# Kernel optimization log

Measured on AMD Instinct MI355X. Metric: run time of the kernel, lower is better.

## Reference

```python
import jax, jax.numpy as jnp
import numpy as np

M_GROUPS = 512  # fixed number of segments (== fill_max for ii)


def setup_inputs() -> dict:
    key = jax.random.key(0)
    ks = jax.random.split(key, 8)
    B, N, D = 4, 16384, 384
    x = jax.random.normal(ks[0], (B, N, D), dtype=jnp.float32)
    ii = jax.random.randint(ks[1], (N,), 0, M_GROUPS)
    s = 1.0 / np.sqrt(D)
    f_w = jax.random.uniform(ks[2], (D, D), jnp.float32, -s, s)
    f_b = jax.random.uniform(ks[3], (D,), jnp.float32, -s, s)
    g_w = jax.random.uniform(ks[4], (D, D), jnp.float32, -s, s)
    g_b = jax.random.uniform(ks[5], (D,), jnp.float32, -s, s)
    h_w = jax.random.uniform(ks[6], (D, D), jnp.float32, -s, s)
    h_b = jax.random.uniform(ks[7], (D,), jnp.float32, -s, s)
    return {"x": x, "ii": ii, "f_w": f_w, "f_b": f_b,
            "g_w": g_w, "g_b": g_b, "h_w": h_w, "h_b": h_b}


def reference(x, ii, f_w, f_b, g_w, g_b, h_w, h_b):
    # x: [B, N, D], ii: [N] group indices in [0, M_GROUPS)
    logits = x @ g_w.T + g_b                      # g(x): [B, N, D]
    exp_logits = jnp.exp(logits)
    # segment sum over n for each group m (== one-hot einsum 'bnm,bnd->bmd')
    seg = lambda e: jax.ops.segment_sum(e, ii, num_segments=M_GROUPS)
    sum_exp = jax.vmap(seg)(exp_logits)           # [B, M, D]
    denom = sum_exp[:, ii]                        # gather back: [B, N, D]
    w = exp_logits / (denom + 1e-6)
    fx = x @ f_w.T + f_b                          # f(x): [B, N, D]
    y = jax.vmap(seg)(fx * w)                     # [B, M, D]
    y = y @ h_w.T + h_b                           # h(y)
    return y[:, ii]                               # expand: [B, N, D]
```

## Files before the change

kernel.cpp:

```cpp
#include <hip/hip_runtime.h>
#include <hip/hip_bf16.h>

#define D 384
#define NROWS 16384
#define BATCH 4
#define MG 512
#define RTOT (BATCH * NROWS)
#define NC (2 * D)
#define JB 64
#define NJB (D / JB)
#define BM 128
#define BK 32
#define NKT (D / BK)
#define NMT (RTOT / BM)

typedef __attribute__((ext_vector_type(8))) short bf16x8;
typedef __attribute__((ext_vector_type(4))) float f32x4;

static __device__ __forceinline__ unsigned short f2bf(float f) {
  unsigned int u = __float_as_uint(f);
  unsigned int r = u + 0x7fffu + ((u >> 16) & 1u);
  return (unsigned short)(r >> 16);
}
static __device__ __forceinline__ unsigned int cvtpk(float lo, float hi) {
  unsigned int r;
  asm("v_cvt_pk_bf16_f32 %0, %1, %2" : "=v"(r) : "v"(lo), "v"(hi));
  return r;
}
static __device__ __forceinline__ float frcp(float f) {
  float r;
  asm("v_rcp_f32 %0, %1" : "=v"(r) : "v"(f));
  return r;
}

typedef __attribute__((address_space(1))) const void gvoid_t;
typedef __attribute__((address_space(3))) void lvoid_t;
static __device__ __forceinline__ void gl16(const void* g, void* l) {
  __builtin_amdgcn_global_load_lds((gvoid_t*)g, (lvoid_t*)l, 16, 0, 0);
}

__global__ void k_build_w(const float* __restrict__ g_w, const float* __restrict__ f_w,
                          const float* __restrict__ h_w,
                          unsigned short* __restrict__ wt2, unsigned short* __restrict__ hw) {
  const int totW = NC * D, totH = D * D;
  int tid0 = blockIdx.x * blockDim.x + threadIdx.x;
  int stride = gridDim.x * blockDim.x;
  for (int idx = tid0; idx < totW; idx += stride) {
    int jblk = idx / (128 * D);
    int rem = idx % (128 * D);
    int c = rem / D, k = rem % D;
    int j = jblk * JB + (c & 63);
    float v = (c < JB) ? g_w[j * D + k] : f_w[j * D + k];
    wt2[idx] = f2bf(v);
  }
  for (int idx = tid0; idx < totH; idx += stride) hw[idx] = f2bf(h_w[idx]);
}

__global__ void k_csr(const int* __restrict__ ii, int* __restrict__ csr_start,
                      int* __restrict__ csr_rows, int* __restrict__ grp_sorted) {
  __shared__ int cnt[MG];
  __shared__ int scan[MG];
  const int t = threadIdx.x;
  cnt[t] = 0;
  __syncthreads();
  for (int n = t; n < NROWS; n += MG) atomicAdd(&cnt[ii[n]], 1);
  __syncthreads();
  const int v = cnt[t];
  scan[t] = v;
  __syncthreads();
#pragma unroll
  for (int o = 1; o < MG; o <<= 1) {
    int u = (t >= o) ? scan[t - o] : 0;
    __syncthreads();
    scan[t] += u;
    __syncthreads();
  }
  const int excl = scan[t] - v;
  csr_start[t] = excl;
  if (t == MG - 1) csr_start[MG] = scan[t];
  cnt[t] = excl;
  __syncthreads();
  for (int n = t; n < NROWS; n += MG) {
    int m = ii[n];
    int pos = atomicAdd(&cnt[m], 1);
    csr_rows[pos] = n;
    grp_sorted[pos] = m;
  }
}

__global__ __launch_bounds__(256, 4) void k_gemm1(
    const float* __restrict__ x, const unsigned short* __restrict__ wt2,
    const float* __restrict__ g_b, const float* __restrict__ f_b,
    const int* __restrict__ csr_rows, const int* __restrict__ grp_sorted,
    float* __restrict__ s1acc, float* __restrict__ s2acc) {
  __shared__ __attribute__((aligned(16))) unsigned short As[2][BM * BK];
  __shared__ __attribute__((aligned(16))) unsigned short Bs[2][BM * BK];
  __shared__ int grpS[BM];

  const int wg = blockIdx.x;
  const int xcd = wg & 7;
  const int ix = wg >> 3;
  const int mt = xcd * (NMT / 8) + ix / NJB;
  const int jb = ix % NJB;
  const int b = mt >> 7;
  const int ib = (mt & 127) * BM;
  const int j0 = jb * JB;

  const int tid = threadIdx.x;
  const int lane = tid & 63, wid = tid >> 6;
  const int wr = wid >> 1, wc = wid & 1;

  if (tid < BM) grpS[tid] = grp_sorted[ib + tid];

  const int srow = wid * 32 + (lane >> 2);
  const int arow0 = b * NROWS + csr_rows[ib + srow];
  const int arow1 = b * NROWS + csr_rows[ib + srow + 16];
  const char* aS0 = (const char*)x + (size_t)arow0 * (D * 4) + (lane & 3) * 32;
  const char* aS1 = (const char*)x + (size_t)arow1 * (D * 4) + (lane & 3) * 32;
  const char* bS0 = (const char*)wt2 + (size_t)jb * (128 * D * 2) + (size_t)srow * (D * 2) +
                    (lane & 3) * 16;
  const char* bS1 = bS0 + 16 * (D * 2);

  f32x4 acc[4][4];
#pragma unroll
  for (int m = 0; m < 4; m++)
#pragma unroll
    for (int n = 0; n < 4; n++) acc[m][n] = (f32x4){0.f, 0.f, 0.f, 0.f};

  float4 a00 = *(const float4*)(aS0);
  float4 a01 = *(const float4*)(aS0 + 16);
  float4 a10 = *(const float4*)(aS1);
  float4 a11 = *(const float4*)(aS1 + 16);
  {
    char* bd = (char*)Bs[0] + wid * 2048;
    gl16(bS0, bd);
    gl16(bS1, bd + 1024);
    int4 p0, p1;
    p0.x = cvtpk(a00.x, a00.y); p0.y = cvtpk(a00.z, a00.w);
    p0.z = cvtpk(a01.x, a01.y); p0.w = cvtpk(a01.z, a01.w);
    p1.x = cvtpk(a10.x, a10.y); p1.y = cvtpk(a10.z, a10.w);
    p1.z = cvtpk(a11.x, a11.y); p1.w = cvtpk(a11.z, a11.w);
    *(int4*)((char*)As[0] + wid * 2048 + lane * 16) = p0;
    *(int4*)((char*)As[0] + wid * 2048 + 1024 + lane * 16) = p1;
  }
  __syncthreads();

#pragma unroll 1
  for (int kt = 0; kt < NKT; ++kt) {
    const int cur = kt & 1;
    const bool more = (kt < NKT - 1);
    if (more) {
      const int kbf = (kt + 1) * (BK * 4);
      const int kbb = (kt + 1) * (BK * 2);
      a00 = *(const float4*)(aS0 + kbf);
      a01 = *(const float4*)(aS0 + kbf + 16);
      a10 = *(const float4*)(aS1 + kbf);
      a11 = *(const float4*)(aS1 + kbf + 16);
      char* bd = (char*)Bs[cur ^ 1] + wid * 2048;
      gl16(bS0 + kbb, bd);
      gl16(bS1 + kbb, bd + 1024);
    }
    bf16x8 af[4], bfv[4];
#pragma unroll
    for (int m = 0; m < 4; m++)
      af[m] = *(const bf16x8*)(&As[cur][(wr * 64 + m * 16 + (lane & 15)) * BK + (lane >> 4) * 8]);
#pragma unroll
    for (int n = 0; n < 4; n++) {
      const int c = (n < 2) ? (wc * 32 + n * 16) : (64 + wc * 32 + (n - 2) * 16);
      bfv[n] = *(const bf16x8*)(&Bs[cur][(c + (lane & 15)) * BK + (lane >> 4) * 8]);
    }
#pragma unroll
    for (int m = 0; m < 4; m++)
#pragma unroll
      for (int n = 0; n < 4; n++)
        acc[m][n] = __builtin_amdgcn_mfma_f32_16x16x32_bf16(af[m], bfv[n], acc[m][n], 0, 0, 0);
    if (more) {
      int4 p0, p1;
      p0.x = cvtpk(a00.x, a00.y); p0.y = cvtpk(a00.z, a00.w);
      p0.z = cvtpk(a01.x, a01.y); p0.w = cvtpk(a01.z, a01.w);
      p1.x = cvtpk(a10.x, a10.y); p1.y = cvtpk(a10.z, a10.w);
      p1.z = cvtpk(a11.x, a11.y); p1.w = cvtpk(a11.z, a11.w);
      *(int4*)((char*)As[cur ^ 1] + wid * 2048 + lane * 16) = p0;
      *(int4*)((char*)As[cur ^ 1] + wid * 2048 + 1024 + lane * 16) = p1;
    }
    __syncthreads();
  }

  const int jc = lane & 15;
  const int jA = j0 + wc * 32 + jc;
  const float gb0 = g_b[jA], gb1 = g_b[jA + 16];
  const float fb0 = f_b[jA], fb1 = f_b[jA + 16];

  int gmr[4][4];
#pragma unroll
  for (int m = 0; m < 4; m++)
#pragma unroll
    for (int r = 0; r < 4; r++)
      gmr[m][r] = grpS[wr * 64 + m * 16 + (lane >> 4) * 4 + r];

#pragma unroll
  for (int m = 0; m < 4; m++)
#pragma unroll
    for (int r = 0; r < 4; r++) {
      const float e0 = expf(acc[m][0][r] + gb0);
      const float e1 = expf(acc[m][1][r] + gb1);
      const float f0 = acc[m][2][r] + fb0;
      const float f1 = acc[m][3][r] + fb1;
      acc[m][0][r] = e0; acc[m][1][r] = e1;
      acc[m][2][r] = f0 * e0; acc[m][3][r] = f1 * e1;
    }

  const int gLo = grpS[wr * 64], gHi = grpS[wr * 64 + 63];
  for (int g = gLo; g <= gHi; ++g) {
    float v0 = 0.f, v1 = 0.f, v2 = 0.f, v3 = 0.f;
#pragma unroll
    for (int m = 0; m < 4; m++)
#pragma unroll
      for (int r = 0; r < 4; r++)
        if (gmr[m][r] == g) {
          v0 += acc[m][0][r]; v1 += acc[m][1][r];
          v2 += acc[m][2][r]; v3 += acc[m][3][r];
        }
    v0 += __shfl_xor(v0, 16); v0 += __shfl_xor(v0, 32);
    v1 += __shfl_xor(v1, 16); v1 += __shfl_xor(v1, 32);
    v2 += __shfl_xor(v2, 16); v2 += __shfl_xor(v2, 32);
    v3 += __shfl_xor(v3, 16); v3 += __shfl_xor(v3, 32);
    if (lane < 16) {
      float* s1p = s1acc + ((size_t)(b * MG + g)) * D + j0 + wc * 32 + lane;
      float* s2p = s2acc + ((size_t)(b * MG + g)) * D + j0 + wc * 32 + lane;
      atomicAdd(s1p, v0);
      atomicAdd(s1p + 16, v1);
      atomicAdd(s2p, v2);
      atomicAdd(s2p + 16, v3);
    }
  }
}

__global__ __launch_bounds__(256) void k_gemm2(
    const float* __restrict__ s1, const float* __restrict__ s2,
    const unsigned short* __restrict__ hw, const float* __restrict__ h_b,
    float* __restrict__ outpre) {
  const int tid = threadIdx.x, lane = tid & 63, wid = tid >> 6;
  const int r0 = blockIdx.y * 16;
  const int c0 = blockIdx.x * 64 + wid * 16;
  f32x4 acc = (f32x4){0.f, 0.f, 0.f, 0.f};
  const int arow = r0 + (lane & 15);
  const float* s1p = s1 + (size_t)arow * D + (lane >> 4) * 8;
  const float* s2p = s2 + (size_t)arow * D + (lane >> 4) * 8;
  const unsigned short* bRow = hw + (size_t)(c0 + (lane & 15)) * D + (lane >> 4) * 8;
#pragma unroll
  for (int kt = 0; kt < D / 32; kt++) {
    float4 u0 = *(const float4*)(s1p + kt * 32);
    float4 u1 = *(const float4*)(s1p + kt * 32 + 4);
    float4 w0 = *(const float4*)(s2p + kt * 32);
    float4 w1 = *(const float4*)(s2p + kt * 32 + 4);
    int4 yi;
    yi.x = cvtpk(w0.x * frcp(u0.x + 1e-6f), w0.y * frcp(u0.y + 1e-6f));
    yi.y = cvtpk(w0.z * frcp(u0.z + 1e-6f), w0.w * frcp(u0.w + 1e-6f));
    yi.z = cvtpk(w1.x * frcp(u1.x + 1e-6f), w1.y * frcp(u1.y + 1e-6f));
    yi.w = cvtpk(w1.z * frcp(u1.z + 1e-6f), w1.w * frcp(u1.w + 1e-6f));
    bf16x8 af = *(bf16x8*)&yi;
    bf16x8 bf_ = *(const bf16x8*)(bRow + kt * 32);
    acc = __builtin_amdgcn_mfma_f32_16x16x32_bf16(af, bf_, acc, 0, 0, 0);
  }
  const int col = c0 + (lane & 15);
  const float hb = h_b[col];
#pragma unroll
  for (int r = 0; r < 4; r++) {
    const int row = r0 + (lane >> 4) * 4 + r;
    outpre[(size_t)row * D + col] = acc[r] + hb;
  }
}

__global__ void k_gather(const float* __restrict__ outpre, const int* __restrict__ ii,
                         float* __restrict__ out) {
  const long total4 = (long)RTOT * (D / 4);
  for (long i = blockIdx.x * (long)blockDim.x + threadIdx.x; i < total4;
       i += (long)gridDim.x * blockDim.x) {
    const long row = i / (D / 4);
    const int q = (int)(i % (D / 4));
    const int b = (int)(row >> 14);
    const int n = (int)(row & (NROWS - 1));
    const int g = ii[n];
    ((float4*)out)[i] = ((const float4*)outpre)[((size_t)(b * MG + g)) * (D / 4) + q];
  }
}

extern "C" void kernel_launch(void* const* d_in, const int* in_sizes, int n_in,
                              void* d_out, int out_size, void* d_ws, size_t ws_size,
                              hipStream_t stream) {
  const float* x = (const float*)d_in[0];
  const int* ii = (const int*)d_in[1];
  const float* f_w = (const float*)d_in[2];
  const float* f_b = (const float*)d_in[3];
  const float* g_w = (const float*)d_in[4];
  const float* g_b = (const float*)d_in[5];
  const float* h_w = (const float*)d_in[6];
  const float* h_b = (const float*)d_in[7];
  float* out = (float*)d_out;

  char* ws = (char*)d_ws;
  size_t off = 0;
  auto alloc = [&](size_t bytes) {
    size_t p = off;
    off = (off + bytes + 255) & ~(size_t)255;
    return p;
  };
  unsigned short* wt2 = (unsigned short*)(ws + alloc((size_t)NC * D * 2));
  unsigned short* hw = (unsigned short*)(ws + alloc((size_t)D * D * 2));
  float* s1acc = (float*)(ws + alloc((size_t)BATCH * MG * D * 4));
  float* s2acc = (float*)(ws + alloc((size_t)BATCH * MG * D * 4));
  float* outpre = (float*)(ws + alloc((size_t)BATCH * MG * D * 4));
  int* csr_start = (int*)(ws + alloc((MG + 1) * 4));
  int* csr_rows = (int*)(ws + alloc((size_t)NROWS * 4));
  int* grp_sorted = (int*)(ws + alloc((size_t)NROWS * 4));

  hipMemsetAsync(s1acc, 0, (size_t)2 * BATCH * MG * D * 4, stream);

  k_build_w<<<dim3(1152), dim3(256), 0, stream>>>(g_w, f_w, h_w, wt2, hw);
  k_csr<<<dim3(1), dim3(MG), 0, stream>>>(ii, csr_start, csr_rows, grp_sorted);
  k_gemm1<<<dim3(NJB * NMT), dim3(256), 0, stream>>>(x, wt2, g_b, f_b, csr_rows,
                                                     grp_sorted, s1acc, s2acc);
  k_gemm2<<<dim3(D / 64, (BATCH * MG) / 16), dim3(256), 0, stream>>>(s1acc, s2acc, hw, h_b,
                                                                     outpre);
  k_gather<<<dim3(4096), dim3(256), 0, stream>>>(outpre, ii, out);
}
```

Baseline: 146.6 us.

## Load GEMM operands directly into registers and merge prep kernels into one launch

The first GEMM no longer stages A and B tiles through LDS with barriers. Each lane now loads its MFMA fragments straight from global memory (fp32 x converted to bf16 in registers), using register double buffering over a fully unrolled K loop, and occupancy is lowered to 2 blocks. The memset, weight conversion and CSR build are also fused into a single k_prep launch using block specialization. The aim is to cut LDS traffic, barrier stalls and launch overhead. The cost is redundant global loads, since each wave reloads A/B fragments that were shared through LDS before, and higher register pressure.

```diff
diff --git a/kernel.cpp b/kernel.cpp
--- a/kernel.cpp
+++ b/kernel.cpp
@@ -10,8 +10,7 @@
 #define JB 64
 #define NJB (D / JB)
 #define BM 128
-#define BK 32
-#define NKT (D / BK)
+#define NKT (D / 32)
 #define NMT (RTOT / BM)
 
 typedef __attribute__((ext_vector_type(8))) short bf16x8;
@@ -33,70 +32,63 @@
   return r;
 }
 
-typedef __attribute__((address_space(1))) const void gvoid_t;
-typedef __attribute__((address_space(3))) void lvoid_t;
-static __device__ __forceinline__ void gl16(const void* g, void* l) {
-  __builtin_amdgcn_global_load_lds((gvoid_t*)g, (lvoid_t*)l, 16, 0, 0);
-}
-
-__global__ void k_build_w(const float* __restrict__ g_w, const float* __restrict__ f_w,
-                          const float* __restrict__ h_w,
-                          unsigned short* __restrict__ wt2, unsigned short* __restrict__ hw) {
-  const int totW = NC * D, totH = D * D;
-  int tid0 = blockIdx.x * blockDim.x + threadIdx.x;
-  int stride = gridDim.x * blockDim.x;
-  for (int idx = tid0; idx < totW; idx += stride) {
-    int jblk = idx / (128 * D);
-    int rem = idx % (128 * D);
-    int c = rem / D, k = rem % D;
-    int j = jblk * JB + (c & 63);
-    float v = (c < JB) ? g_w[j * D + k] : f_w[j * D + k];
-    wt2[idx] = f2bf(v);
-  }
-  for (int idx = tid0; idx < totH; idx += stride) hw[idx] = f2bf(h_w[idx]);
-}
-
-__global__ void k_csr(const int* __restrict__ ii, int* __restrict__ csr_start,
-                      int* __restrict__ csr_rows, int* __restrict__ grp_sorted) {
+__global__ __launch_bounds__(512) void k_prep(
+    const int* __restrict__ ii, const float* __restrict__ g_w,
+    const float* __restrict__ f_w, const float* __restrict__ h_w,
+    unsigned short* __restrict__ wt2, unsigned short* __restrict__ hw,
+    int* __restrict__ csr_rows, int* __restrict__ grp_sorted,
+    float* __restrict__ s12) {
   __shared__ int cnt[MG];
   __shared__ int scan[MG];
+  const int blk = blockIdx.x;
   const int t = threadIdx.x;
-  cnt[t] = 0;
-  __syncthreads();
-  for (int n = t; n < NROWS; n += MG) atomicAdd(&cnt[ii[n]], 1);
-  __syncthreads();
-  const int v = cnt[t];
-  scan[t] = v;
-  __syncthreads();
-#pragma unroll
-  for (int o = 1; o < MG; o <<= 1) {
-    int u = (t >= o) ? scan[t - o] : 0;
-    __syncthreads();
-    scan[t] += u;
-    __syncthreads();
-  }
-  const int excl = scan[t] - v;
-  csr_start[t] = excl;
-  if (t == MG - 1) csr_start[MG] = scan[t];
-  cnt[t] = excl;
-  __syncthreads();
-  for (int n = t; n < NROWS; n += MG) {
-    int m = ii[n];
-    int pos = atomicAdd(&cnt[m], 1);
-    csr_rows[pos] = n;
-    grp_sorted[pos] = m;
-  }
-}
-
-__global__ __launch_bounds__(256, 4) void k_gemm1(
+  if (blk == 0) {
+    cnt[t] = 0;
+    __syncthreads();
+    for (int n = t; n < NROWS; n += MG) atomicAdd(&cnt[ii[n]], 1);
+    __syncthreads();
+    const int v = cnt[t];
+    scan[t] = v;
+    __syncthreads();
+#pragma unroll
+    for (int o = 1; o < MG; o <<= 1) {
+      int u = (t >= o) ? scan[t - o] : 0;
+      __syncthreads();
+      scan[t] += u;
+      __syncthreads();
+    }
+    cnt[t] = scan[t] - v;
+    __syncthreads();
+    for (int n = t; n < NROWS; n += MG) {
+      int m = ii[n];
+      int pos = atomicAdd(&cnt[m], 1);
+      csr_rows[pos] = n;
+      grp_sorted[pos] = m;
+    }
+  } else if (blk < 64) {
+    const int tot4 = 2 * BATCH * MG * D / 4;
+    float4 z = {0.f, 0.f, 0.f, 0.f};
+    for (int i = (blk - 1) * 512 + t; i < tot4; i += 63 * 512) ((float4*)s12)[i] = z;
+  } else {
+    const int tid0 = (blk - 64) * 512 + t;
+    const int stride = 64 * 512;
+    for (int idx = tid0; idx < NC * D; idx += stride) {
+      int jblk = idx / (128 * D);
+      int rem = idx % (128 * D);
+      int c = rem / D, k = rem % D;
+      int j = jblk * JB + (c & 63);
+      float v = (c < JB) ? g_w[j * D + k] : f_w[j * D + k];
+      wt2[idx] = f2bf(v);
+    }
+    for (int idx = tid0; idx < D * D; idx += stride) hw[idx] = f2bf(h_w[idx]);
+  }
+}
+
+__global__ __launch_bounds__(256, 2) void k_gemm1(
     const float* __restrict__ x, const unsigned short* __restrict__ wt2,
     const float* __restrict__ g_b, const float* __restrict__ f_b,
     const int* __restrict__ csr_rows, const int* __restrict__ grp_sorted,
     float* __restrict__ s1acc, float* __restrict__ s2acc) {
-  __shared__ __attribute__((aligned(16))) unsigned short As[2][BM * BK];
-  __shared__ __attribute__((aligned(16))) unsigned short Bs[2][BM * BK];
-  __shared__ int grpS[BM];
-
   const int wg = blockIdx.x;
   const int xcd = wg & 7;
   const int ix = wg >> 3;
@@ -110,16 +102,18 @@
   const int lane = tid & 63, wid = tid >> 6;
   const int wr = wid >> 1, wc = wid & 1;
 
-  if (tid < BM) grpS[tid] = grp_sorted[ib + tid];
-
-  const int srow = wid * 32 + (lane >> 2);
-  const int arow0 = b * NROWS + csr_rows[ib + srow];
-  const int arow1 = b * NROWS + csr_rows[ib + srow + 16];
-  const char* aS0 = (const char*)x + (size_t)arow0 * (D * 4) + (lane & 3) * 32;
-  const char* aS1 = (const char*)x + (size_t)arow1 * (D * 4) + (lane & 3) * 32;
-  const char* bS0 = (const char*)wt2 + (size_t)jb * (128 * D * 2) + (size_t)srow * (D * 2) +
-                    (lane & 3) * 16;
-  const char* bS1 = bS0 + 16 * (D * 2);
+  const float* aP[4];
+#pragma unroll
+  for (int m = 0; m < 4; m++) {
+    const int r = csr_rows[ib + wr * 64 + m * 16 + (lane & 15)];
+    aP[m] = x + (size_t)(b * NROWS + r) * D + (lane >> 4) * 8;
+  }
+  const unsigned short* bP[4];
+#pragma unroll
+  for (int n = 0; n < 4; n++) {
+    const int c = (n < 2) ? (wc * 32 + n * 16) : (64 + wc * 32 + (n - 2) * 16);
+    bP[n] = wt2 + (size_t)jb * (128 * D) + (size_t)(c + (lane & 15)) * D + (lane >> 4) * 8;
+  }
 
   f32x4 acc[4][4];
 #pragma unroll
@@ -127,67 +121,44 @@
 #pragma unroll
     for (int n = 0; n < 4; n++) acc[m][n] = (f32x4){0.f, 0.f, 0.f, 0.f};
 
-  float4 a00 = *(const float4*)(aS0);
-  float4 a01 = *(const float4*)(aS0 + 16);
-  float4 a10 = *(const float4*)(aS1);
-  float4 a11 = *(const float4*)(aS1 + 16);
-  {
-    char* bd = (char*)Bs[0] + wid * 2048;
-    gl16(bS0, bd);
-    gl16(bS1, bd + 1024);
-    int4 p0, p1;
-    p0.x = cvtpk(a00.x, a00.y); p0.y = cvtpk(a00.z, a00.w);
-    p0.z = cvtpk(a01.x, a01.y); p0.w = cvtpk(a01.z, a01.w);
-    p1.x = cvtpk(a10.x, a10.y); p1.y = cvtpk(a10.z, a10.w);
-    p1.z = cvtpk(a11.x, a11.y); p1.w = cvtpk(a11.z, a11.w);
-    *(int4*)((char*)As[0] + wid * 2048 + lane * 16) = p0;
-    *(int4*)((char*)As[0] + wid * 2048 + 1024 + lane * 16) = p1;
-  }
-  __syncthreads();
-
-#pragma unroll 1
-  for (int kt = 0; kt < NKT; ++kt) {
-    const int cur = kt & 1;
-    const bool more = (kt < NKT - 1);
-    if (more) {
-      const int kbf = (kt + 1) * (BK * 4);
-      const int kbb = (kt + 1) * (BK * 2);
-      a00 = *(const float4*)(aS0 + kbf);
-      a01 = *(const float4*)(aS0 + kbf + 16);
-      a10 = *(const float4*)(aS1 + kbf);
-      a11 = *(const float4*)(aS1 + kbf + 16);
-      char* bd = (char*)Bs[cur ^ 1] + wid * 2048;
-      gl16(bS0 + kbb, bd);
-      gl16(bS1 + kbb, bd + 1024);
-    }
-    bf16x8 af[4], bfv[4];
-#pragma unroll
-    for (int m = 0; m < 4; m++)
-      af[m] = *(const bf16x8*)(&As[cur][(wr * 64 + m * 16 + (lane & 15)) * BK + (lane >> 4) * 8]);
-#pragma unroll
-    for (int n = 0; n < 4; n++) {
-      const int c = (n < 2) ? (wc * 32 + n * 16) : (64 + wc * 32 + (n - 2) * 16);
-      bfv[n] = *(const bf16x8*)(&Bs[cur][(c + (lane & 15)) * BK + (lane >> 4) * 8]);
-    }
-#pragma unroll
-    for (int m = 0; m < 4; m++)
-#pragma unroll
-      for (int n = 0; n < 4; n++)
-        acc[m][n] = __builtin_amdgcn_mfma_f32_16x16x32_bf16(af[m], bfv[n], acc[m][n], 0, 0, 0);
-    if (more) {
-      int4 p0, p1;
-      p0.x = cvtpk(a00.x, a00.y); p0.y = cvtpk(a00.z, a00.w);
-      p0.z = cvtpk(a01.x, a01.y); p0.w = cvtpk(a01.z, a01.w);
-      p1.x = cvtpk(a10.x, a10.y); p1.y = cvtpk(a10.z, a10.w);
-      p1.z = cvtpk(a11.x, a11.y); p1.w = cvtpk(a11.z, a11.w);
-      *(int4*)((char*)As[cur ^ 1] + wid * 2048 + lane * 16) = p0;
-      *(int4*)((char*)As[cur ^ 1] + wid * 2048 + 1024 + lane * 16) = p1;
-    }
-    __syncthreads();
-  }
-
-  const int jc = lane & 15;
-  const int jA = j0 + wc * 32 + jc;
+  float4 Alo0[4], Ahi0[4], Alo1[4], Ahi1[4];
+  bf16x8 B0[4], B1[4];
+
+#define LOADA(L, H, kt)                                                                  \
+  _Pragma("unroll") for (int m = 0; m < 4; m++) {                                        \
+    L[m] = *(const float4*)(aP[m] + (kt) * 32);                                          \
+    H[m] = *(const float4*)(aP[m] + (kt) * 32 + 4);                                      \
+  }
+#define LOADB(Bv, kt)                                                                    \
+  _Pragma("unroll") for (int n = 0; n < 4; n++) Bv[n] =                                  \
+      *(const bf16x8*)(bP[n] + (kt) * 32);
+#define STEP(L, H, Bv)                                                                   \
+  _Pragma("unroll") for (int m = 0; m < 4; m++) {                                        \
+    int4 p;                                                                              \
+    p.x = cvtpk(L[m].x, L[m].y);                                                         \
+    p.y = cvtpk(L[m].z, L[m].w);                                                         \
+    p.z = cvtpk(H[m].x, H[m].y);                                                         \
+    p.w = cvtpk(H[m].z, H[m].w);                                                         \
+    bf16x8 af = *(bf16x8*)&p;                                                            \
+    _Pragma("unroll") for (int n = 0; n < 4; n++) acc[m][n] =                            \
+        __builtin_amdgcn_mfma_f32_16x16x32_bf16(af, Bv[n], acc[m][n], 0, 0, 0);          \
+  }
+
+  LOADA(Alo0, Ahi0, 0)
+  LOADB(B0, 0)
+#pragma unroll
+  for (int kt = 0; kt < NKT; kt += 2) {
+    LOADA(Alo1, Ahi1, kt + 1)
+    LOADB(B1, kt + 1)
+    STEP(Alo0, Ahi0, B0)
+    if (kt + 2 < NKT) {
+      LOADA(Alo0, Ahi0, kt + 2)
+      LOADB(B0, kt + 2)
+    }
+    STEP(Alo1, Ahi1, B1)
+  }
+
+  const int jA = j0 + wc * 32 + (lane & 15);
   const float gb0 = g_b[jA], gb1 = g_b[jA + 16];
   const float fb0 = f_b[jA], fb1 = f_b[jA + 16];
 
@@ -196,7 +167,7 @@
   for (int m = 0; m < 4; m++)
 #pragma unroll
     for (int r = 0; r < 4; r++)
-      gmr[m][r] = grpS[wr * 64 + m * 16 + (lane >> 4) * 4 + r];
+      gmr[m][r] = grp_sorted[ib + wr * 64 + m * 16 + (lane >> 4) * 4 + r];
 
 #pragma unroll
   for (int m = 0; m < 4; m++)
@@ -210,7 +181,7 @@
       acc[m][2][r] = f0 * e0; acc[m][3][r] = f1 * e1;
     }
 
-  const int gLo = grpS[wr * 64], gHi = grpS[wr * 64 + 63];
+  const int gLo = grp_sorted[ib + wr * 64], gHi = grp_sorted[ib + wr * 64 + 63];
   for (int g = gLo; g <= gHi; ++g) {
     float v0 = 0.f, v1 = 0.f, v2 = 0.f, v3 = 0.f;
 #pragma unroll
@@ -311,14 +282,11 @@
   float* s1acc = (float*)(ws + alloc((size_t)BATCH * MG * D * 4));
   float* s2acc = (float*)(ws + alloc((size_t)BATCH * MG * D * 4));
   float* outpre = (float*)(ws + alloc((size_t)BATCH * MG * D * 4));
-  int* csr_start = (int*)(ws + alloc((MG + 1) * 4));
   int* csr_rows = (int*)(ws + alloc((size_t)NROWS * 4));
   int* grp_sorted = (int*)(ws + alloc((size_t)NROWS * 4));
 
-  hipMemsetAsync(s1acc, 0, (size_t)2 * BATCH * MG * D * 4, stream);
-
-  k_build_w<<<dim3(1152), dim3(256), 0, stream>>>(g_w, f_w, h_w, wt2, hw);
-  k_csr<<<dim3(1), dim3(MG), 0, stream>>>(ii, csr_start, csr_rows, grp_sorted);
+  k_prep<<<dim3(128), dim3(512), 0, stream>>>(ii, g_w, f_w, h_w, wt2, hw, csr_rows,
+                                              grp_sorted, s1acc);
   k_gemm1<<<dim3(NJB * NMT), dim3(256), 0, stream>>>(x, wt2, g_b, f_b, csr_rows,
                                                      grp_sorted, s1acc, s2acc);
   k_gemm2<<<dim3(D / 64, (BATCH * MG) / 16), dim3(256), 0, stream>>>(s1acc, s2acc, hw, h_b,
```

After: 276.6 us. +88.7%, slower.
